# Kernel tuning notes

Measured on AMD Instinct MI355X. Metric: run time of the kernel, lower is better.

## Reference

```python
import jax, jax.numpy as jnp
import numpy as np


def setup_inputs() -> dict:
    key = jax.random.key(0)
    k1, k2, k3 = jax.random.split(key, 3)
    B, S, D_IN, D_OUT = 4, 2048, 4096, 16384
    x = jax.random.normal(k1, (B, S, D_IN), dtype=jnp.float32)
    # xavier_normal-ish init scaled by 0.1, as in the torch module
    std = 0.1 * (2.0 / (D_IN + D_OUT)) ** 0.5
    weight = jax.random.normal(k2, (D_OUT, D_IN), dtype=jnp.float32) * std
    bias = jax.random.normal(k3, (D_OUT,), dtype=jnp.float32) * 0.01
    return {"x": x, "weight": weight, "bias": bias}


def reference(x, weight, bias):
    input_dtype = x.dtype
    x_f32 = x.astype(jnp.float32)
    w_f32 = jnp.clip(weight.astype(jnp.float32), -2.0, 2.0)
    gamma = jnp.maximum(jnp.mean(jnp.abs(w_f32)), 1e-4)          # scalar scale
    w_quant = jnp.clip(jnp.round(w_f32 / gamma), -1.0, 1.0)      # ternary {-1,0,1}
    w_deq = w_quant * gamma
    # straight-through estimator: forward uses w_deq, gradient flows to w_f32
    w_ste = w_f32 + jax.lax.stop_gradient(w_deq - w_f32)
    out = jnp.einsum('bsi,oi->bso', x_f32, w_ste) + bias.astype(jnp.float32)
    return out.astype(input_dtype)
```

## Files before the change

kernel.cpp:

```cpp
#include <hip/hip_runtime.h>

#define M_DIM 8192
#define K_DIM 4096
#define N_DIM 16384
#define NW_ELEMS (16384 * 4096)
#define NX_ELEMS (8192 * 4096)
#define NT 32

typedef int int4x __attribute__((ext_vector_type(4)));


__global__ void zero_scalars(double* g, int* xm) {
    if (threadIdx.x == 0 && blockIdx.x == 0) { *g = 0.0; *xm = 0; }
}

__global__ void gamma_reduce(const float4* __restrict__ w4, double* __restrict__ gsum, int n4) {
    double acc = 0.0;
    int stride = gridDim.x * blockDim.x;
    for (int i = blockIdx.x * blockDim.x + threadIdx.x; i < n4; i += stride) {
        float4 v = w4[i];
        float s = fminf(fabsf(v.x), 2.0f) + fminf(fabsf(v.y), 2.0f) +
                  fminf(fabsf(v.z), 2.0f) + fminf(fabsf(v.w), 2.0f);
        acc += (double)s;
    }
    int lane = threadIdx.x & 63;
    int wid = threadIdx.x >> 6;
    #pragma unroll
    for (int off = 32; off > 0; off >>= 1) acc += __shfl_down(acc, off, 64);
    __shared__ double sred[4];
    if (lane == 0) sred[wid] = acc;
    __syncthreads();
    if (threadIdx.x == 0) atomicAdd(gsum, sred[0] + sred[1] + sred[2] + sred[3]);
}

__global__ void xmax_reduce(const float4* __restrict__ x4, int* __restrict__ xmb, int n4) {
    float m = 0.0f;
    int stride = gridDim.x * blockDim.x;
    for (int i = blockIdx.x * blockDim.x + threadIdx.x; i < n4; i += stride) {
        float4 v = x4[i];
        m = fmaxf(m, fmaxf(fmaxf(fabsf(v.x), fabsf(v.y)), fmaxf(fabsf(v.z), fabsf(v.w))));
    }
    int lane = threadIdx.x & 63;
    int wid = threadIdx.x >> 6;
    #pragma unroll
    for (int off = 32; off > 0; off >>= 1) m = fmaxf(m, __shfl_down(m, off, 64));
    __shared__ float sred[4];
    if (lane == 0) sred[wid] = m;
    __syncthreads();
    if (threadIdx.x == 0) {
        float bm = fmaxf(fmaxf(sred[0], sred[1]), fmaxf(sred[2], sred[3]));
        atomicMax(xmb, __float_as_int(bm));
    }
}


__global__ void quant_w(const float4* __restrict__ w4, int4x* __restrict__ wq,
                        const double* __restrict__ gsum) {
    double gamma = fmax(*gsum * (1.0 / (double)NW_ELEMS), 1e-4);
    double rg = 1.0 / gamma;
    int i = blockIdx.x * blockDim.x + threadIdx.x;
    signed char b[16];
    #pragma unroll
    for (int k = 0; k < 4; ++k) {
        float4 v = w4[4 * i + k];
        float vals[4] = {v.x, v.y, v.z, v.w};
        #pragma unroll
        for (int j = 0; j < 4; ++j) {
            float cv = fminf(fmaxf(vals[j], -2.0f), 2.0f);
            double t = rint((double)cv * rg);
            t = fmax(-1.0, fmin(1.0, t));
            b[4 * k + j] = (signed char)(int)t;
        }
    }
    int4x o;
    __builtin_memcpy(&o, b, 16);
    wq[i] = o;
}


__global__ void quant_x(const float4* __restrict__ x4, int4x* __restrict__ xq,
                        const int* __restrict__ xmb) {
    const float s = 127.0f / __int_as_float(*xmb);
    int i = blockIdx.x * blockDim.x + threadIdx.x;
    signed char b[16];
    #pragma unroll
    for (int k = 0; k < 4; ++k) {
        float4 v = x4[4 * i + k];
        float vals[4] = {v.x, v.y, v.z, v.w};
        #pragma unroll
        for (int j = 0; j < 4; ++j) {
            int q = (int)rintf(vals[j] * s);
            q = max(-127, min(127, q));
            b[4 * k + j] = (signed char)q;
        }
    }
    int4x o;
    __builtin_memcpy(&o, b, 16);
    xq[i] = o;
}


__device__ inline void gload16(const char* g, char* lds) {
    __builtin_amdgcn_global_load_lds((const __attribute__((address_space(1))) void*)g,
        (__attribute__((address_space(3))) void*)lds, 16, 0, 0);
}

#define MFMAI8(a, b, c) __builtin_amdgcn_mfma_i32_16x16x64_i8(a, b, c, 0, 0, 0)

__global__ __launch_bounds__(512, 2) void gemm_kernel(
    const char* __restrict__ A,
    const char* __restrict__ B,
    const float* __restrict__ bias,
    const double* __restrict__ gsum,
    const int* __restrict__ xmb,
    float* __restrict__ out) {
    __shared__ __align__(16) char sm[131072];

    const int tid = threadIdx.x;
    const int wid = tid >> 6;
    const int lane = tid & 63;
    const int fr = lane & 15;
    const int kg = lane >> 4;
    const int f7 = fr & 7;
    const int wm = wid >> 2;
    const int wn = wid & 3;

    const int orig = blockIdx.x;
    const int bm = ((orig & 7) << 2) + ((orig >> 3) & 3);
    const int bn = orig >> 5;
    const int m0 = bm << 8, n0 = bn << 8;

    const int srow = tid >> 3;
    const int ks16 = (((tid & 7) ^ (srow & 7)) << 4);
    const int poff = srow * K_DIM + ks16;
    const char* Ab = A + (size_t)m0 * K_DIM + poff;
    const char* Bb = B + (size_t)n0 * K_DIM + poff;
    const uint32_t dwave = (uint32_t)(wid << 10);

    #define STAGE_A(ktB, bufb) do {                                             \
        _Pragma("unroll")                                                       \
        for (int _i = 0; _i < 4; ++_i)                                          \
            gload16(Ab + (_i * (64 * K_DIM) + (ktB)),                           \
                    sm + (bufb) * 32768 + (_i << 13) + dwave);                  \
    } while (0)
    #define STAGE_B(ktB, bufb) do {                                             \
        _Pragma("unroll")                                                       \
        for (int _i = 0; _i < 4; ++_i)                                          \
            gload16(Bb + (_i * (64 * K_DIM) + (ktB)),                           \
                    sm + 65536 + (bufb) * 32768 + (_i << 13) + dwave);          \
    } while (0)

    const char* const smc = sm;
    const char* const pAk0 = smc + ((wm * 128 + fr) << 7) + ((kg ^ f7) << 4);
    const char* const pAk1 = smc + ((wm * 128 + fr) << 7) + (((4 | kg) ^ f7) << 4);
    const char* const pBk0 = smc + 65536 + ((wn * 64 + fr) << 7) + ((kg ^ f7) << 4);
    const char* const pBk1 = smc + 65536 + ((wn * 64 + fr) << 7) + (((4 | kg) ^ f7) << 4);

    int4x acc[8][4] = {};
    int4x a0[4][2], a1[4][2], b0[2][2], b1[2][2];

    STAGE_A(0, 0); STAGE_B(0, 0);
    STAGE_A(128, 1); STAGE_B(128, 1);
    asm volatile("s_waitcnt vmcnt(8)" ::: "memory");
    __builtin_amdgcn_s_barrier();
    asm volatile("" ::: "memory");
    __builtin_amdgcn_sched_barrier(0);
    #pragma unroll
    for (int i = 0; i < 4; ++i) {
        a0[i][0] = *(const int4x*)(pAk0 + i * 2048);
        a0[i][1] = *(const int4x*)(pAk1 + i * 2048);
    }

    #define TILE(T_, CUR_, NXT_) do {                                             \
        const int _kt2 = ((T_) + 2) << 7;                                         \
        const bool _st = ((T_) < NT - 2);                                         \
        const bool _rd = ((T_) < NT - 1);                                         \
                                   \
        _Pragma("unroll")                                                         \
        for (int j = 0; j < 2; ++j) {                                             \
            b0[j][0] = *(const int4x*)(pBk0 + ((CUR_) * 32768 + j * 2048));       \
            b0[j][1] = *(const int4x*)(pBk1 + ((CUR_) * 32768 + j * 2048));       \
        }                                                                         \
        _Pragma("unroll")                                                         \
        for (int i = 0; i < 4; ++i) {                                             \
            a1[i][0] = *(const int4x*)(pAk0 + ((CUR_) * 32768 + (4 + i) * 2048)); \
            a1[i][1] = *(const int4x*)(pAk1 + ((CUR_) * 32768 + (4 + i) * 2048)); \
        }                                                                         \
        __builtin_amdgcn_s_setprio(1);                                            \
        _Pragma("unroll")                                                         \
        for (int i = 0; i < 4; ++i)                                               \
            _Pragma("unroll")                                                     \
            for (int j = 0; j < 2; ++j) {                                         \
                acc[i][j] = MFMAI8(a0[i][0], b0[j][0], acc[i][j]);                \
                acc[i][j] = MFMAI8(a0[i][1], b0[j][1], acc[i][j]);                \
            }                                                                     \
        __builtin_amdgcn_s_setprio(0);                                            \
                                             \
        _Pragma("unroll")                                                         \
        for (int j = 0; j < 2; ++j) {                                             \
            b1[j][0] = *(const int4x*)(pBk0 + ((CUR_) * 32768 + (2 + j) * 2048)); \
            b1[j][1] = *(const int4x*)(pBk1 + ((CUR_) * 32768 + (2 + j) * 2048)); \
        }                                                                         \
        __builtin_amdgcn_s_setprio(1);                                            \
        _Pragma("unroll")                                                         \
        for (int i = 0; i < 4; ++i)                                               \
            _Pragma("unroll")                                                     \
            for (int j = 0; j < 2; ++j) {                                         \
                acc[i][2 + j] = MFMAI8(a0[i][0], b1[j][0], acc[i][2 + j]);        \
                acc[i][2 + j] = MFMAI8(a0[i][1], b1[j][1], acc[i][2 + j]);        \
            }                                                                     \
        __builtin_amdgcn_s_setprio(0);                                            \
            \
        asm volatile("s_waitcnt vmcnt(4) lgkmcnt(0)" ::: "memory");               \
        __builtin_amdgcn_sched_barrier(0);                                        \
        __builtin_amdgcn_s_barrier();                                             \
        asm volatile("" ::: "memory");                                            \
        __builtin_amdgcn_sched_barrier(0);                                        \
              \
        if (_st) STAGE_A(_kt2, CUR_);                                             \
        if (_rd) {                                                                \
            _Pragma("unroll")                                                     \
            for (int i = 0; i < 4; ++i) {                                         \
                a0[i][0] = *(const int4x*)(pAk0 + ((NXT_) * 32768 + i * 2048));   \
                a0[i][1] = *(const int4x*)(pAk1 + ((NXT_) * 32768 + i * 2048));   \
            }                                                                     \
        }                                                                         \
        __builtin_amdgcn_s_setprio(1);                                            \
        _Pragma("unroll")                                                         \
        for (int i = 0; i < 4; ++i)                                               \
            _Pragma("unroll")                                                     \
            for (int j = 0; j < 2; ++j) {                                         \
                acc[4 + i][j] = MFMAI8(a1[i][0], b0[j][0], acc[4 + i][j]);        \
                acc[4 + i][j] = MFMAI8(a1[i][1], b0[j][1], acc[4 + i][j]);        \
            }                                                                     \
        __builtin_amdgcn_s_setprio(0);                                            \
        if (_st) STAGE_B(_kt2, CUR_);                                             \
        __builtin_amdgcn_s_setprio(1);                                            \
        _Pragma("unroll")                                                         \
        for (int i = 0; i < 4; ++i)                                               \
            _Pragma("unroll")                                                     \
            for (int j = 0; j < 2; ++j) {                                         \
                acc[4 + i][2 + j] = MFMAI8(a1[i][0], b1[j][0], acc[4 + i][2 + j]);\
                acc[4 + i][2 + j] = MFMAI8(a1[i][1], b1[j][1], acc[4 + i][2 + j]);\
            }                                                                     \
        __builtin_amdgcn_s_setprio(0);                                            \
                                    \
        if (_st) {                                                                \
            asm volatile("s_waitcnt vmcnt(8)" ::: "memory");                      \
        } else if ((T_) == NT - 2) {                                              \
            asm volatile("s_waitcnt vmcnt(0)" ::: "memory");                      \
        }                                                                         \
        __builtin_amdgcn_sched_barrier(0);                                        \
        __builtin_amdgcn_s_barrier();                                             \
        asm volatile("" ::: "memory");                                            \
        __builtin_amdgcn_sched_barrier(0);                                        \
    } while (0)

    for (int t = 0; t < NT; t += 2) {
        TILE(t, 0, 1);
        TILE(t + 1, 1, 0);
    }

    const double gamma = fmax(*gsum * (1.0 / (double)NW_ELEMS), 1e-4);
    const float scale = (float)(gamma * (double)__int_as_float(*xmb) * (1.0 / 127.0));
    const int rbase = m0 + wm * 128 + (kg << 2);
    #pragma unroll
    for (int j = 0; j < 4; ++j) {
        const int gn = n0 + wn * 64 + j * 16 + fr;
        const float bv = bias[gn];
        #pragma unroll
        for (int i = 0; i < 8; ++i) {
            #pragma unroll
            for (int jj = 0; jj < 4; ++jj) {
                const int gm = rbase + i * 16 + jj;
                out[(size_t)gm * N_DIM + gn] = (float)acc[i][j][jj] * scale + bv;
            }
        }
    }
}


extern "C" void kernel_launch(void* const* d_in, const int* in_sizes, int n_in,
                              void* d_out, int out_size, void* d_ws, size_t ws_size,
                              hipStream_t stream) {
    const float* x = (const float*)d_in[0];
    const float* w = (const float*)d_in[1];
    const float* bias = (const float*)d_in[2];
    float* out = (float*)d_out;

    char* ws = (char*)d_ws;
    double* gsum = (double*)ws;
    int* xmb = (int*)(ws + 8);
    char* xq = ws + 256;
    char* wq = ws + 256 + (size_t)NX_ELEMS;

    zero_scalars<<<1, 1, 0, stream>>>(gsum, xmb);
    gamma_reduce<<<2048, 256, 0, stream>>>((const float4*)w, gsum, NW_ELEMS / 4);
    xmax_reduce<<<2048, 256, 0, stream>>>((const float4*)x, xmb, NX_ELEMS / 4);
    quant_w<<<NW_ELEMS / 16 / 256, 256, 0, stream>>>((const float4*)w, (int4x*)wq, gsum);
    quant_x<<<NX_ELEMS / 16 / 256, 256, 0, stream>>>((const float4*)x, (int4x*)xq, xmb);

    const int nblk = (M_DIM / 256) * (N_DIM / 256);
    gemm_kernel<<<nblk, 512, 0, stream>>>(xq, wq, bias, gsum, xmb, out);
}
```

Before: 720.5 us.

## Merge prep kernels and reschedule GEMM main loop into barrier-delimited MFMA phases

```diff
diff --git a/kernel.cpp b/kernel.cpp
--- a/kernel.cpp
+++ b/kernel.cpp
@@ -14,89 +14,86 @@
     if (threadIdx.x == 0 && blockIdx.x == 0) { *g = 0.0; *xm = 0; }
 }
 
-__global__ void gamma_reduce(const float4* __restrict__ w4, double* __restrict__ gsum, int n4) {
-    double acc = 0.0;
-    int stride = gridDim.x * blockDim.x;
-    for (int i = blockIdx.x * blockDim.x + threadIdx.x; i < n4; i += stride) {
-        float4 v = w4[i];
-        float s = fminf(fabsf(v.x), 2.0f) + fminf(fabsf(v.y), 2.0f) +
-                  fminf(fabsf(v.z), 2.0f) + fminf(fabsf(v.w), 2.0f);
-        acc += (double)s;
-    }
-    int lane = threadIdx.x & 63;
-    int wid = threadIdx.x >> 6;
-    #pragma unroll
-    for (int off = 32; off > 0; off >>= 1) acc += __shfl_down(acc, off, 64);
-    __shared__ double sred[4];
-    if (lane == 0) sred[wid] = acc;
-    __syncthreads();
-    if (threadIdx.x == 0) atomicAdd(gsum, sred[0] + sred[1] + sred[2] + sred[3]);
-}
-
-__global__ void xmax_reduce(const float4* __restrict__ x4, int* __restrict__ xmb, int n4) {
-    float m = 0.0f;
-    int stride = gridDim.x * blockDim.x;
-    for (int i = blockIdx.x * blockDim.x + threadIdx.x; i < n4; i += stride) {
-        float4 v = x4[i];
-        m = fmaxf(m, fmaxf(fmaxf(fabsf(v.x), fabsf(v.y)), fmaxf(fabsf(v.z), fabsf(v.w))));
-    }
-    int lane = threadIdx.x & 63;
-    int wid = threadIdx.x >> 6;
-    #pragma unroll
-    for (int off = 32; off > 0; off >>= 1) m = fmaxf(m, __shfl_down(m, off, 64));
-    __shared__ float sred[4];
-    if (lane == 0) sred[wid] = m;
-    __syncthreads();
-    if (threadIdx.x == 0) {
-        float bm = fmaxf(fmaxf(sred[0], sred[1]), fmaxf(sred[2], sred[3]));
-        atomicMax(xmb, __float_as_int(bm));
-    }
-}
-
-
-__global__ void quant_w(const float4* __restrict__ w4, int4x* __restrict__ wq,
-                        const double* __restrict__ gsum) {
-    double gamma = fmax(*gsum * (1.0 / (double)NW_ELEMS), 1e-4);
-    double rg = 1.0 / gamma;
-    int i = blockIdx.x * blockDim.x + threadIdx.x;
-    signed char b[16];
-    #pragma unroll
-    for (int k = 0; k < 4; ++k) {
-        float4 v = w4[4 * i + k];
-        float vals[4] = {v.x, v.y, v.z, v.w};
-        #pragma unroll
-        for (int j = 0; j < 4; ++j) {
-            float cv = fminf(fmaxf(vals[j], -2.0f), 2.0f);
-            double t = rint((double)cv * rg);
-            t = fmax(-1.0, fmin(1.0, t));
-            b[4 * k + j] = (signed char)(int)t;
-        }
-    }
-    int4x o;
-    __builtin_memcpy(&o, b, 16);
-    wq[i] = o;
-}
-
-
-__global__ void quant_x(const float4* __restrict__ x4, int4x* __restrict__ xq,
-                        const int* __restrict__ xmb) {
-    const float s = 127.0f / __int_as_float(*xmb);
-    int i = blockIdx.x * blockDim.x + threadIdx.x;
-    signed char b[16];
-    #pragma unroll
-    for (int k = 0; k < 4; ++k) {
-        float4 v = x4[4 * i + k];
-        float vals[4] = {v.x, v.y, v.z, v.w};
-        #pragma unroll
-        for (int j = 0; j < 4; ++j) {
-            int q = (int)rintf(vals[j] * s);
-            q = max(-127, min(127, q));
-            b[4 * k + j] = (signed char)q;
-        }
-    }
-    int4x o;
-    __builtin_memcpy(&o, b, 16);
-    xq[i] = o;
+__global__ void reduce_both(const float4* __restrict__ w4, const float4* __restrict__ x4,
+                            double* __restrict__ gsum, int* __restrict__ xmb) {
+    const int lane = threadIdx.x & 63;
+    const int wid = threadIdx.x >> 6;
+    if (blockIdx.x < 2048) {
+        double acc = 0.0;
+        const int stride = 2048 * 256;
+        for (int i = blockIdx.x * 256 + threadIdx.x; i < NW_ELEMS / 4; i += stride) {
+            float4 v = w4[i];
+            float s = fminf(fabsf(v.x), 2.0f) + fminf(fabsf(v.y), 2.0f) +
+                      fminf(fabsf(v.z), 2.0f) + fminf(fabsf(v.w), 2.0f);
+            acc += (double)s;
+        }
+        #pragma unroll
+        for (int off = 32; off > 0; off >>= 1) acc += __shfl_down(acc, off, 64);
+        __shared__ double sred[4];
+        if (lane == 0) sred[wid] = acc;
+        __syncthreads();
+        if (threadIdx.x == 0) atomicAdd(gsum, sred[0] + sred[1] + sred[2] + sred[3]);
+    } else {
+        float m = 0.0f;
+        const int stride = 1024 * 256;
+        for (int i = (blockIdx.x - 2048) * 256 + threadIdx.x; i < NX_ELEMS / 4; i += stride) {
+            float4 v = x4[i];
+            m = fmaxf(m, fmaxf(fmaxf(fabsf(v.x), fabsf(v.y)), fmaxf(fabsf(v.z), fabsf(v.w))));
+        }
+        #pragma unroll
+        for (int off = 32; off > 0; off >>= 1) m = fmaxf(m, __shfl_down(m, off, 64));
+        __shared__ float fred[4];
+        if (lane == 0) fred[wid] = m;
+        __syncthreads();
+        if (threadIdx.x == 0) {
+            float bm = fmaxf(fmaxf(fred[0], fred[1]), fmaxf(fred[2], fred[3]));
+            atomicMax(xmb, __float_as_int(bm));
+        }
+    }
+}
+
+__global__ void quant_both(const float4* __restrict__ w4, int4x* __restrict__ wq,
+                           const float4* __restrict__ x4, int4x* __restrict__ xq,
+                           const double* __restrict__ gsum, const int* __restrict__ xmb) {
+    if (blockIdx.x < 16384) {
+        double gamma = fmax(*gsum * (1.0 / (double)NW_ELEMS), 1e-4);
+        double rg = 1.0 / gamma;
+        int i = blockIdx.x * 256 + threadIdx.x;
+        signed char b[16];
+        #pragma unroll
+        for (int k = 0; k < 4; ++k) {
+            float4 v = w4[4 * i + k];
+            float vals[4] = {v.x, v.y, v.z, v.w};
+            #pragma unroll
+            for (int j = 0; j < 4; ++j) {
+                float cv = fminf(fmaxf(vals[j], -2.0f), 2.0f);
+                double t = rint((double)cv * rg);
+                t = fmax(-1.0, fmin(1.0, t));
+                b[4 * k + j] = (signed char)(int)t;
+            }
+        }
+        int4x o;
+        __builtin_memcpy(&o, b, 16);
+        wq[i] = o;
+    } else {
+        const float s = 127.0f / __int_as_float(*xmb);
+        int i = (blockIdx.x - 16384) * 256 + threadIdx.x;
+        signed char b[16];
+        #pragma unroll
+        for (int k = 0; k < 4; ++k) {
+            float4 v = x4[4 * i + k];
+            float vals[4] = {v.x, v.y, v.z, v.w};
+            #pragma unroll
+            for (int j = 0; j < 4; ++j) {
+                int q = (int)rintf(vals[j] * s);
+                q = max(-127, min(127, q));
+                b[4 * k + j] = (signed char)q;
+            }
+        }
+        int4x o;
+        __builtin_memcpy(&o, b, 16);
+        xq[i] = o;
+    }
 }
 
 
@@ -106,6 +103,19 @@
 }
 
 #define MFMAI8(a, b, c) __builtin_amdgcn_mfma_i32_16x16x64_i8(a, b, c, 0, 0, 0)
+
+#define PH_ENTER() do {                                                         \
+    __builtin_amdgcn_s_barrier();                                               \
+    asm volatile("s_waitcnt lgkmcnt(0)" ::: "memory");                          \
+    __builtin_amdgcn_sched_barrier(0);                                          \
+    __builtin_amdgcn_s_setprio(1);                                              \
+} while (0)
+#define PH_EXIT() do {                                                          \
+    __builtin_amdgcn_s_setprio(0);                                              \
+    __builtin_amdgcn_s_barrier();                                               \
+    asm volatile("" ::: "memory");                                              \
+    __builtin_amdgcn_sched_barrier(0);                                          \
+} while (0)
 
 __global__ __launch_bounds__(512, 2) void gemm_kernel(
     const char* __restrict__ A,
@@ -170,38 +180,39 @@
         a0[i][0] = *(const int4x*)(pAk0 + i * 2048);
         a0[i][1] = *(const int4x*)(pAk1 + i * 2048);
     }
+    #pragma unroll
+    for (int j = 0; j < 2; ++j) {
+        b0[j][0] = *(const int4x*)(pBk0 + j * 2048);
+        b0[j][1] = *(const int4x*)(pBk1 + j * 2048);
+    }
 
     #define TILE(T_, CUR_, NXT_) do {                                             \
         const int _kt2 = ((T_) + 2) << 7;                                         \
         const bool _st = ((T_) < NT - 2);                                         \
         const bool _rd = ((T_) < NT - 1);                                         \
-                                   \
+                           \
         _Pragma("unroll")                                                         \
         for (int j = 0; j < 2; ++j) {                                             \
-            b0[j][0] = *(const int4x*)(pBk0 + ((CUR_) * 32768 + j * 2048));       \
-            b0[j][1] = *(const int4x*)(pBk1 + ((CUR_) * 32768 + j * 2048));       \
+            b1[j][0] = *(const int4x*)(pBk0 + ((CUR_) * 32768 + (2 + j) * 2048)); \
+            b1[j][1] = *(const int4x*)(pBk1 + ((CUR_) * 32768 + (2 + j) * 2048)); \
         }                                                                         \
+        PH_ENTER();                                                               \
+        _Pragma("unroll")                                                         \
+        for (int i = 0; i < 4; ++i)                                               \
+            _Pragma("unroll")                                                     \
+            for (int j = 0; j < 2; ++j) {                                         \
+                acc[i][j] = MFMAI8(a0[i][0], b0[j][0], acc[i][j]);                \
+                acc[i][j] = MFMAI8(a0[i][1], b0[j][1], acc[i][j]);                \
+            }                                                                     \
+        PH_EXIT();                                                                \
+             \
         _Pragma("unroll")                                                         \
         for (int i = 0; i < 4; ++i) {                                             \
             a1[i][0] = *(const int4x*)(pAk0 + ((CUR_) * 32768 + (4 + i) * 2048)); \
             a1[i][1] = *(const int4x*)(pAk1 + ((CUR_) * 32768 + (4 + i) * 2048)); \
         }                                                                         \
-        __builtin_amdgcn_s_setprio(1);                                            \
-        _Pragma("unroll")                                                         \
-        for (int i = 0; i < 4; ++i)                                               \
-            _Pragma("unroll")                                                     \
-            for (int j = 0; j < 2; ++j) {                                         \
-                acc[i][j] = MFMAI8(a0[i][0], b0[j][0], acc[i][j]);                \
-                acc[i][j] = MFMAI8(a0[i][1], b0[j][1], acc[i][j]);                \
-            }                                                                     \
-        __builtin_amdgcn_s_setprio(0);                                            \
-                                             \
-        _Pragma("unroll")                                                         \
-        for (int j = 0; j < 2; ++j) {                                             \
-            b1[j][0] = *(const int4x*)(pBk0 + ((CUR_) * 32768 + (2 + j) * 2048)); \
-            b1[j][1] = *(const int4x*)(pBk1 + ((CUR_) * 32768 + (2 + j) * 2048)); \
-        }                                                                         \
-        __builtin_amdgcn_s_setprio(1);                                            \
+        if (_st) STAGE_B(_kt2, CUR_);                                             \
+        PH_ENTER();                                                               \
         _Pragma("unroll")                                                         \
         for (int i = 0; i < 4; ++i)                                               \
             _Pragma("unroll")                                                     \
@@ -209,23 +220,10 @@
                 acc[i][2 + j] = MFMAI8(a0[i][0], b1[j][0], acc[i][2 + j]);        \
                 acc[i][2 + j] = MFMAI8(a0[i][1], b1[j][1], acc[i][2 + j]);        \
             }                                                                     \
-        __builtin_amdgcn_s_setprio(0);                                            \
-            \
-        asm volatile("s_waitcnt vmcnt(4) lgkmcnt(0)" ::: "memory");               \
-        __builtin_amdgcn_sched_barrier(0);                                        \
-        __builtin_amdgcn_s_barrier();                                             \
-        asm volatile("" ::: "memory");                                            \
-        __builtin_amdgcn_sched_barrier(0);                                        \
-              \
+        PH_EXIT();                                                                \
+                   \
         if (_st) STAGE_A(_kt2, CUR_);                                             \
-        if (_rd) {                                                                \
-            _Pragma("unroll")                                                     \
-            for (int i = 0; i < 4; ++i) {                                         \
-                a0[i][0] = *(const int4x*)(pAk0 + ((NXT_) * 32768 + i * 2048));   \
-                a0[i][1] = *(const int4x*)(pAk1 + ((NXT_) * 32768 + i * 2048));   \
-            }                                                                     \
-        }                                                                         \
-        __builtin_amdgcn_s_setprio(1);                                            \
+        PH_ENTER();                                                               \
         _Pragma("unroll")                                                         \
         for (int i = 0; i < 4; ++i)                                               \
             _Pragma("unroll")                                                     \
@@ -234,17 +232,6 @@
                 acc[4 + i][j] = MFMAI8(a1[i][1], b0[j][1], acc[4 + i][j]);        \
             }                                                                     \
         __builtin_amdgcn_s_setprio(0);                                            \
-        if (_st) STAGE_B(_kt2, CUR_);                                             \
-        __builtin_amdgcn_s_setprio(1);                                            \
-        _Pragma("unroll")                                                         \
-        for (int i = 0; i < 4; ++i)                                               \
-            _Pragma("unroll")                                                     \
-            for (int j = 0; j < 2; ++j) {                                         \
-                acc[4 + i][2 + j] = MFMAI8(a1[i][0], b1[j][0], acc[4 + i][2 + j]);\
-                acc[4 + i][2 + j] = MFMAI8(a1[i][1], b1[j][1], acc[4 + i][2 + j]);\
-            }                                                                     \
-        __builtin_amdgcn_s_setprio(0);                                            \
-                                    \
         if (_st) {                                                                \
             asm volatile("s_waitcnt vmcnt(8)" ::: "memory");                      \
         } else if ((T_) == NT - 2) {                                              \
@@ -254,6 +241,28 @@
         __builtin_amdgcn_s_barrier();                                             \
         asm volatile("" ::: "memory");                                            \
         __builtin_amdgcn_sched_barrier(0);                                        \
+                  \
+        if (_rd) {                                                                \
+            _Pragma("unroll")                                                     \
+            for (int i = 0; i < 4; ++i) {                                         \
+                a0[i][0] = *(const int4x*)(pAk0 + ((NXT_) * 32768 + i * 2048));   \
+                a0[i][1] = *(const int4x*)(pAk1 + ((NXT_) * 32768 + i * 2048));   \
+            }                                                                     \
+            _Pragma("unroll")                                                     \
+            for (int j = 0; j < 2; ++j) {                                         \
+                b0[j][0] = *(const int4x*)(pBk0 + ((NXT_) * 32768 + j * 2048));   \
+                b0[j][1] = *(const int4x*)(pBk1 + ((NXT_) * 32768 + j * 2048));   \
+            }                                                                     \
+        }                                                                         \
+        PH_ENTER();                                                               \
+        _Pragma("unroll")                                                         \
+        for (int i = 0; i < 4; ++i)                                               \
+            _Pragma("unroll")                                                     \
+            for (int j = 0; j < 2; ++j) {                                         \
+                acc[4 + i][2 + j] = MFMAI8(a1[i][0], b1[j][0], acc[4 + i][2 + j]);\
+                acc[4 + i][2 + j] = MFMAI8(a1[i][1], b1[j][1], acc[4 + i][2 + j]);\
+            }                                                                     \
+        PH_EXIT();                                                                \
     } while (0)
 
     for (int t = 0; t < NT; t += 2) {
@@ -295,10 +304,9 @@
     char* wq = ws + 256 + (size_t)NX_ELEMS;
 
     zero_scalars<<<1, 1, 0, stream>>>(gsum, xmb);
-    gamma_reduce<<<2048, 256, 0, stream>>>((const float4*)w, gsum, NW_ELEMS / 4);
-    xmax_reduce<<<2048, 256, 0, stream>>>((const float4*)x, xmb, NX_ELEMS / 4);
-    quant_w<<<NW_ELEMS / 16 / 256, 256, 0, stream>>>((const float4*)w, (int4x*)wq, gsum);
-    quant_x<<<NX_ELEMS / 16 / 256, 256, 0, stream>>>((const float4*)x, (int4x*)xq, xmb);
+    reduce_both<<<3072, 256, 0, stream>>>((const float4*)w, (const float4*)x, gsum, xmb);
+    quant_both<<<24576, 256, 0, stream>>>((const float4*)w, (int4x*)wq,
+                                          (const float4*)x, (int4x*)xq, gsum, xmb);
 
     const int nblk = (M_DIM / 256) * (N_DIM / 256);
     gemm_kernel<<<nblk, 512, 0, stream>>>(xq, wq, bias, gsum, xmb, out);
```

Result: slower. 779.4 us (+8.2%).
